# Kernel optimization log

Hardware: AMD Instinct MI355X
Metric: run time of the kernel (lower is better)

Reference implementation:

```python
import jax, jax.numpy as jnp
import numpy as np

B, N, M = 8, 4096, 77
Q_DIM, CTX_DIM = 1024, 768
H, D = 16, 64
INNER = H * D  # 1024


def setup_inputs() -> dict:
    key = jax.random.key(0)
    ks = jax.random.split(key, 7)
    x = jax.random.normal(ks[0], (B, N, Q_DIM), dtype=jnp.float32)
    context = jax.random.normal(ks[1], (B, M, CTX_DIM), dtype=jnp.float32)
    # Linear weights stored as [in, out] so y = x @ W (no bias for q/k/v).
    Wq = jax.random.normal(ks[2], (Q_DIM, INNER), dtype=jnp.float32) * (Q_DIM ** -0.5)
    Wk = jax.random.normal(ks[3], (CTX_DIM, INNER), dtype=jnp.float32) * (CTX_DIM ** -0.5)
    Wv = jax.random.normal(ks[4], (CTX_DIM, INNER), dtype=jnp.float32) * (CTX_DIM ** -0.5)
    Wo = jax.random.normal(ks[5], (INNER, Q_DIM), dtype=jnp.float32) * (INNER ** -0.5)
    bo = jax.random.normal(ks[6], (Q_DIM,), dtype=jnp.float32) * 0.01
    return {"x": x, "context": context, "Wq": Wq, "Wk": Wk, "Wv": Wv, "Wo": Wo, "bo": bo}


def reference(x, context, Wq, Wk, Wv, Wo, bo):
    scale = D ** -0.5
    # Project and split heads: [B, S, H*D] -> [B, H, S, D]
    def heads(t):
        b, s, _ = t.shape
        return t.reshape(b, s, H, D).transpose(0, 2, 1, 3)
    q = heads(x @ Wq)        # [B, H, N, D]
    k = heads(context @ Wk)  # [B, H, M, D]
    v = heads(context @ Wv)  # [B, H, M, D]
    scores = jnp.einsum('bhid,bhjd->bhij', q, k) * scale  # [B, H, N, M]
    attn = jax.nn.softmax(scores, axis=-1)
    out = jnp.einsum('bhij,bhjd->bhid', attn, v)          # [B, H, N, D]
    out = out.transpose(0, 2, 1, 3).reshape(x.shape[0], x.shape[1], INNER)
    return out @ Wo + bo  # dropout p=0.0 -> identity
```

## Files before the change

kernel.cpp:

```cpp
#include <hip/hip_runtime.h>
#include <hip/hip_bf16.h>

typedef _Float16 f16x8 __attribute__((ext_vector_type(8)));
typedef float f32x4 __attribute__((ext_vector_type(4)));

#define MFMA16(a, b, c) __builtin_amdgcn_mfma_f32_16x16x32_f16(a, b, c, 0, 0, 0)

__device__ __forceinline__ void load_lds16(const void* g, void* l) {
  __builtin_amdgcn_global_load_lds(
      (__attribute__((address_space(1))) void*)g,
      (__attribute__((address_space(3))) void*)l, 16, 0, 0);
}

__global__ __launch_bounds__(256) void k_cvt16(const float* __restrict__ in,
                                               _Float16* __restrict__ out, int n8) {
  int stride = gridDim.x * blockDim.x;
  for (int i = blockIdx.x * blockDim.x + threadIdx.x; i < n8; i += stride) {
    const float4* p = (const float4*)(in + (size_t)i * 8);
    float4 a = p[0], b = p[1];
    f16x8 v = {(_Float16)a.x, (_Float16)a.y, (_Float16)a.z, (_Float16)a.w,
               (_Float16)b.x, (_Float16)b.y, (_Float16)b.z, (_Float16)b.w};
    *(f16x8*)(out + (size_t)i * 8) = v;
  }
}

__global__ __launch_bounds__(256) void k_transpose(const float* __restrict__ in,
                                                   _Float16* __restrict__ out, int K, int N) {
  __shared__ float tile[64][65];
  int k0 = blockIdx.y * 64, n0 = blockIdx.x * 64;
  int t = threadIdx.x;
  {
    int nn = t & 63, kb = t >> 6;
#pragma unroll
    for (int i = 0; i < 16; ++i) {
      int kk = kb + i * 4;
      tile[kk][nn] = in[(size_t)(k0 + kk) * N + n0 + nn];
    }
  }
  __syncthreads();
  {
    int kk = t & 63, nb = t >> 6;
#pragma unroll
    for (int i = 0; i < 16; ++i) {
      int nn = nb + i * 4;
      out[(size_t)(n0 + nn) * K + k0 + kk] = (_Float16)tile[kk][nn];
    }
  }
}

__global__ __launch_bounds__(64) void k_kvproj(const _Float16* __restrict__ ctxh,
                                               const _Float16* __restrict__ Wkt,
                                               const _Float16* __restrict__ Wvt,
                                               _Float16* __restrict__ Kg,
                                               _Float16* __restrict__ Vtg) {
  int mt = blockIdx.x, nt = blockIdx.y;
  int lane = threadIdx.x;
  int l15 = lane & 15, lhi = lane >> 4;
  int arow = mt * 16 + l15;
  if (arow > 615) arow = 615;
  const _Float16* ap = ctxh + (size_t)arow * 768 + lhi * 8;
  const _Float16* kp = Wkt + (size_t)(nt * 16 + l15) * 768 + lhi * 8;
  const _Float16* vp = Wvt + (size_t)(nt * 16 + l15) * 768 + lhi * 8;
  f32x4 ak = {0.f, 0.f, 0.f, 0.f}, av = {0.f, 0.f, 0.f, 0.f};
#pragma unroll 4
  for (int ks = 0; ks < 24; ++ks) {
    f16x8 a = *(const f16x8*)(ap + ks * 32);
    f16x8 bk = *(const f16x8*)(kp + ks * 32);
    f16x8 bv = *(const f16x8*)(vp + ks * 32);
    ak = MFMA16(a, bk, ak);
    av = MFMA16(a, bv, av);
  }
  int n = nt * 16 + l15, h = n >> 6, d = n & 63;
#pragma unroll
  for (int j = 0; j < 4; ++j) {
    int gm = mt * 16 + lhi * 4 + j;
    if (gm < 616) {
      int b = gm / 77, m = gm - b * 77;
      Kg[((size_t)(b * 16 + h) * 77 + m) * 64 + d] = (_Float16)ak[j];
      Vtg[((size_t)(b * 16 + h) * 64 + d) * 128 + m] = (_Float16)av[j];
    }
  }
}

__global__ __launch_bounds__(256) void k_attn(const _Float16* __restrict__ Qh,
                                              const _Float16* __restrict__ Kg,
                                              const _Float16* __restrict__ Vtg,
                                              _Float16* __restrict__ Out) {
  __shared__ __align__(16) char Kl[80 * 128];
  __shared__ __align__(16) char Vl[64 * 256];
  __shared__ __align__(16) char Pl[4 * 16 * 256];
  int bh = blockIdx.y, b = bh >> 4, h = bh & 15;
  int t = threadIdx.x, wid = t >> 6, lane = t & 63;
  int l15 = lane & 15, lhi = lane >> 4;

  const _Float16* Kgp = Kg + (size_t)bh * (77 * 64);
  const _Float16* Vgp = Vtg + (size_t)bh * (64 * 128);

  for (int idx = t; idx < 640; idx += 256) {
    int m = idx >> 3, c = (idx & 7) * 8;
    f16x8 v = {};
    if (m < 77) v = *(const f16x8*)(Kgp + m * 64 + c);
    *(f16x8*)(Kl + ((m * 128 + c * 2) ^ ((m & 7) << 4))) = v;
  }
  for (int idx = t; idx < 1024; idx += 256) {
    int d = idx >> 4, c = (idx & 15) * 8;
    f16x8 v = *(const f16x8*)(Vgp + d * 128 + c);
    *(f16x8*)(Vl + ((d * 256 + c * 2) ^ ((d & 7) << 4))) = v;
  }
  char* myP = Pl + wid * 4096;
#pragma unroll
  for (int i = 0; i < 4; ++i) *(f16x8*)(myP + lane * 64 + i * 16) = f16x8{};
  __syncthreads();

  int qrow = b * 4096 + blockIdx.x * 64 + wid * 16 + l15;
  const _Float16* qp = Qh + (size_t)qrow * 1024 + h * 64 + lhi * 8;
  f16x8 q0 = *(const f16x8*)qp;
  f16x8 q1 = *(const f16x8*)(qp + 32);

  float e[5][4];
  float mx[4] = {-1e30f, -1e30f, -1e30f, -1e30f};
#pragma unroll
  for (int ct = 0; ct < 5; ++ct) {
    int m = ct * 16 + l15;
    int d0b = lhi * 16;
    f16x8 k0 = *(const f16x8*)(Kl + ((m * 128 + d0b) ^ ((m & 7) << 4)));
    f16x8 k1 = *(const f16x8*)(Kl + ((m * 128 + 64 + d0b) ^ ((m & 7) << 4)));
    f32x4 acc = {0.f, 0.f, 0.f, 0.f};
    acc = MFMA16(q0, k0, acc);
    acc = MFMA16(q1, k1, acc);
    bool valid = m < 77;
#pragma unroll
    for (int j = 0; j < 4; ++j) {
      float v = valid ? acc[j] * 0.125f : -1e30f;
      e[ct][j] = v;
      mx[j] = fmaxf(mx[j], v);
    }
  }
#pragma unroll
  for (int off = 1; off < 16; off <<= 1)
#pragma unroll
    for (int j = 0; j < 4; ++j) mx[j] = fmaxf(mx[j], __shfl_xor(mx[j], off, 64));
  float sm[4] = {0.f, 0.f, 0.f, 0.f};
#pragma unroll
  for (int ct = 0; ct < 5; ++ct)
#pragma unroll
    for (int j = 0; j < 4; ++j) {
      float ev = __expf(e[ct][j] - mx[j]);
      e[ct][j] = ev;
      sm[j] += ev;
    }
#pragma unroll
  for (int off = 1; off < 16; off <<= 1)
#pragma unroll
    for (int j = 0; j < 4; ++j) sm[j] += __shfl_xor(sm[j], off, 64);
  float rs[4];
#pragma unroll
  for (int j = 0; j < 4; ++j) rs[j] = 1.0f / sm[j];

#pragma unroll
  for (int ct = 0; ct < 5; ++ct) {
    int m = ct * 16 + l15;
#pragma unroll
    for (int j = 0; j < 4; ++j) {
      int r = lhi * 4 + j;
      *(_Float16*)(myP + ((r * 256 + m * 2) ^ ((r & 7) << 4))) =
          (_Float16)(e[ct][j] * rs[j]);
    }
  }

  f32x4 o[4] = {{0.f,0.f,0.f,0.f},{0.f,0.f,0.f,0.f},{0.f,0.f,0.f,0.f},{0.f,0.f,0.f,0.f}};
#pragma unroll
  for (int ks = 0; ks < 3; ++ks) {
    int m0b = ks * 64 + lhi * 16;
    f16x8 pa = *(const f16x8*)(myP + ((l15 * 256 + m0b) ^ ((l15 & 7) << 4)));
#pragma unroll
    for (int dt = 0; dt < 4; ++dt) {
      int d = dt * 16 + l15;
      f16x8 vb = *(const f16x8*)(Vl + ((d * 256 + m0b) ^ ((d & 7) << 4)));
      o[dt] = MFMA16(pa, vb, o[dt]);
    }
  }
  _Float16* op = Out + (size_t)(b * 4096 + blockIdx.x * 64 + wid * 16) * 1024 + h * 64;
#pragma unroll
  for (int dt = 0; dt < 4; ++dt)
#pragma unroll
    for (int j = 0; j < 4; ++j) {
      int r = lhi * 4 + j;
      op[(size_t)r * 1024 + dt * 16 + l15] = (_Float16)o[dt][j];
    }
}

template <int FINAL>
__global__ __launch_bounds__(512, 2) void k_gemm6(const _Float16* __restrict__ A,
                                                  const _Float16* __restrict__ Bt,
                                                  void* __restrict__ Cout,
                                                  const float* __restrict__ bias,
                                                  int M, int N, int K) {
  __shared__ __align__(16) char lds[131072];
  const int t = threadIdx.x, wid = t >> 6, lane = t & 63;
  const int wr = wid >> 2, wc = wid & 3;
  const int l15 = lane & 15, lhi = lane >> 4;

  int nwg = gridDim.x, bid = blockIdx.x;
  int wg = ((nwg & 7) == 0) ? ((bid & 7) * (nwg >> 3) + (bid >> 3)) : bid;
  const int nTN = N >> 8;
  const int tm = wg / nTN, tn = wg % nTN;

  const _Float16* Ag = A + (size_t)tm * 256 * K;
  const _Float16* Bg = Bt + (size_t)tn * 256 * K;
  const size_t stg = (size_t)(wid * 8 + (lane >> 3)) * K +
                     (size_t)(((lane & 7) ^ ((lane >> 3) & 7)) * 8);
  const int dstg = wid * 1024;

  const int x7 = l15 & 7;
  const int cs0 = (lhi ^ x7) << 4;
  const int cs1 = ((4 + lhi) ^ x7) << 4;
  const int aoff = wr * 16384 + l15 * 128;
  const int boff = 32768 + wc * 8192 + l15 * 128;

  f32x4 acc[8][4];
#pragma unroll
  for (int i = 0; i < 8; ++i)
#pragma unroll
    for (int j = 0; j < 4; ++j) acc[i][j] = f32x4{0.f, 0.f, 0.f, 0.f};
  f16x8 a[4][2], b0[2][2], b1[2][2];

#define STG_A(T, RB) load_lds16(Ag + stg + (size_t)(RB) * K + (T) * 64, \
                                lds + ((T) & 1) * 65536 + (RB) * 128 + dstg)
#define STG_B(T, RB) load_lds16(Bg + stg + (size_t)(RB) * K + (T) * 64, \
                                lds + ((T) & 1) * 65536 + 32768 + (RB) * 128 + dstg)
#define RD_A(BUF, MH) { const int p_ = (BUF) * 65536 + aoff + (MH) * 8192;              \
    _Pragma("unroll") for (int mf = 0; mf < 4; ++mf) {                                  \
      a[mf][0] = *(const f16x8*)&lds[p_ + mf * 2048 + cs0];                             \
      a[mf][1] = *(const f16x8*)&lds[p_ + mf * 2048 + cs1]; } }
#define RD_B(BUF, NH, BREG) { const int q_ = (BUF) * 65536 + boff + (NH) * 4096;        \
    _Pragma("unroll") for (int nf = 0; nf < 2; ++nf) {                                  \
      BREG[nf][0] = *(const f16x8*)&lds[q_ + nf * 2048 + cs0];                          \
      BREG[nf][1] = *(const f16x8*)&lds[q_ + nf * 2048 + cs1]; } }
#define MM(MH, NH, BREG) { __builtin_amdgcn_s_setprio(1);                               \
    _Pragma("unroll") for (int mf = 0; mf < 4; ++mf)                                    \
      _Pragma("unroll") for (int nf = 0; nf < 2; ++nf)                                  \
        _Pragma("unroll") for (int kk = 0; kk < 2; ++kk)                                \
          acc[(MH)*4+mf][(NH)*2+nf] = MFMA16(a[mf][kk], BREG[nf][kk],                   \
                                             acc[(MH)*4+mf][(NH)*2+nf]);                \
    __builtin_amdgcn_s_setprio(0); }
#define VM6 asm volatile("s_waitcnt vmcnt(6)" ::: "memory")
#define VM0 asm volatile("s_waitcnt vmcnt(0)" ::: "memory")
#define BAR __builtin_amdgcn_s_barrier()

  const int nT = K >> 6;

  STG_A(0, 0); STG_A(0, 64); STG_A(0, 128); STG_A(0, 192);
  STG_B(0, 0); STG_B(0, 64); STG_B(0, 128); STG_B(0, 192);
  STG_A(1, 0); STG_A(1, 128);
  STG_B(1, 0); STG_B(1, 64); STG_B(1, 128); STG_B(1, 192);
  asm volatile("s_waitcnt vmcnt(6)" ::: "memory");
  BAR;

  const int nPair = (nT - 2) >> 1;
  for (int i = 0; i < nPair; ++i) {
    const int t0 = 2 * i;
    RD_B(0, 0, b0); RD_A(0, 0); STG_A(t0 + 1, 64); STG_A(t0 + 1, 192); BAR; MM(0, 0, b0); BAR;
    RD_B(0, 1, b1); STG_A(t0 + 2, 0); STG_A(t0 + 2, 128); BAR; MM(0, 1, b1); BAR;
    RD_A(0, 1); STG_B(t0 + 2, 0); STG_B(t0 + 2, 64); BAR; MM(1, 1, b1); BAR;
    STG_B(t0 + 2, 128); STG_B(t0 + 2, 192); VM6; BAR; MM(1, 0, b0); BAR;
    RD_B(1, 0, b0); RD_A(1, 0); STG_A(t0 + 2, 64); STG_A(t0 + 2, 192); BAR; MM(0, 0, b0); BAR;
    RD_B(1, 1, b1); STG_A(t0 + 3, 0); STG_A(t0 + 3, 128); BAR; MM(0, 1, b1); BAR;
    RD_A(1, 1); STG_B(t0 + 3, 0); STG_B(t0 + 3, 64); BAR; MM(1, 1, b1); BAR;
    STG_B(t0 + 3, 128); STG_B(t0 + 3, 192); VM6; BAR; MM(1, 0, b0); BAR;
  }
  RD_B(0, 0, b0); RD_A(0, 0); STG_A(nT - 1, 64); STG_A(nT - 1, 192); BAR; MM(0, 0, b0); BAR;
  RD_B(0, 1, b1); BAR; MM(0, 1, b1); BAR;
  RD_A(0, 1); BAR; MM(1, 1, b1); BAR;
  VM0; BAR; MM(1, 0, b0); BAR;
  RD_B(1, 0, b0); RD_A(1, 0); BAR; MM(0, 0, b0); BAR;
  RD_B(1, 1, b1); BAR; MM(0, 1, b1); BAR;
  RD_A(1, 1); BAR; MM(1, 1, b1); BAR;
  MM(1, 0, b0);

  const long rbase = (long)tm * 256 + wr * 128;
  const int cbase = tn * 256 + wc * 64;
#pragma unroll
  for (int mf = 0; mf < 8; ++mf)
#pragma unroll
    for (int nf = 0; nf < 4; ++nf) {
      int c = cbase + nf * 16 + l15;
      float bv = FINAL ? bias[c] : 0.f;
#pragma unroll
      for (int j = 0; j < 4; ++j) {
        long r = rbase + mf * 16 + lhi * 4 + j;
        float v = acc[mf][nf][j];
        if (FINAL) ((float*)Cout)[r * N + c] = v + bv;
        else ((_Float16*)Cout)[r * N + c] = (_Float16)v;
      }
    }
#undef STG_A
#undef STG_B
#undef RD_A
#undef RD_B
#undef MM
#undef VM6
#undef VM0
#undef BAR
}

extern "C" void kernel_launch(void* const* d_in, const int* in_sizes, int n_in,
                              void* d_out, int out_size, void* d_ws, size_t ws_size,
                              hipStream_t stream) {
  const float* x   = (const float*)d_in[0];
  const float* ctx = (const float*)d_in[1];
  const float* Wq  = (const float*)d_in[2];
  const float* Wk  = (const float*)d_in[3];
  const float* Wv  = (const float*)d_in[4];
  const float* Wo  = (const float*)d_in[5];
  const float* bo  = (const float*)d_in[6];

  char* ws = (char*)d_ws;
  _Float16* xh   = (_Float16*)(ws + 0);
  _Float16* Wqt  = (_Float16*)(ws + 67108864);
  _Float16* Wkt  = (_Float16*)(ws + 69206016);
  _Float16* Wvt  = (_Float16*)(ws + 70778880);
  _Float16* Wot  = (_Float16*)(ws + 72351744);
  _Float16* ctxh = (_Float16*)(ws + 74448896);
  _Float16* Kg   = (_Float16*)(ws + 75395072);
  _Float16* Vtg  = (_Float16*)(ws + 76656640);
  _Float16* Qh   = (_Float16*)d_out;

  k_cvt16<<<4096, 256, 0, stream>>>(x, xh, 33554432 / 8);
  k_cvt16<<<231, 256, 0, stream>>>(ctx, ctxh, 473088 / 8);
  k_transpose<<<dim3(16, 16), 256, 0, stream>>>(Wq, Wqt, 1024, 1024);
  k_transpose<<<dim3(16, 12), 256, 0, stream>>>(Wk, Wkt, 768, 1024);
  k_transpose<<<dim3(16, 12), 256, 0, stream>>>(Wv, Wvt, 768, 1024);
  k_transpose<<<dim3(16, 16), 256, 0, stream>>>(Wo, Wot, 1024, 1024);
  hipMemsetAsync(Vtg, 0, 2097152, stream);
  k_kvproj<<<dim3(39, 64), 64, 0, stream>>>(ctxh, Wkt, Wvt, Kg, Vtg);
  k_gemm6<0><<<dim3(512), dim3(512), 0, stream>>>(xh, Wqt, (void*)Qh, nullptr, 32768, 1024, 1024);
  k_attn<<<dim3(64, 128), 256, 0, stream>>>(Qh, Kg, Vtg, xh);
  k_gemm6<1><<<dim3(512), dim3(512), 0, stream>>>(xh, Wot, d_out, bo, 32768, 1024, 1024);
}
```

Measured before the change: 289.7 us.

## Restructure GEMM main loop: one barrier per tile, split-K register fragments

Replaces the GEMM's finely interleaved schedule, which placed a barrier around every MFMA quarter, with a simpler per-tile schedule. Each tile now does a single vmcnt(0) wait plus barrier, issues the whole next-tile prefetch at once, and interleaves LDS fragment reads (split by k-half) with MFMA groups. The aim is to cut barrier overhead and let LDS reads overlap MFMAs within a wave. In exchange, global prefetch is less spread out, the full wait for the next tile may expose load latency, and the extra fragment registers add register pressure.

```diff
diff --git a/kernel.cpp b/kernel.cpp
--- a/kernel.cpp
+++ b/kernel.cpp
@@ -191,7 +191,7 @@
 }
 
 template <int FINAL>
-__global__ __launch_bounds__(512, 2) void k_gemm6(const _Float16* __restrict__ A,
+__global__ __launch_bounds__(512, 2) void k_gemm7(const _Float16* __restrict__ A,
                                                   const _Float16* __restrict__ Bt,
                                                   void* __restrict__ Cout,
                                                   const float* __restrict__ bias,
@@ -223,60 +223,56 @@
   for (int i = 0; i < 8; ++i)
 #pragma unroll
     for (int j = 0; j < 4; ++j) acc[i][j] = f32x4{0.f, 0.f, 0.f, 0.f};
-  f16x8 a[4][2], b0[2][2], b1[2][2];
+  f16x8 a0k0[4], a0k1[4], a1k0[4], a1k1[4];
+  f16x8 b00[2], b01[2], b10[2], b11[2];
 
 #define STG_A(T, RB) load_lds16(Ag + stg + (size_t)(RB) * K + (T) * 64, \
                                 lds + ((T) & 1) * 65536 + (RB) * 128 + dstg)
 #define STG_B(T, RB) load_lds16(Bg + stg + (size_t)(RB) * K + (T) * 64, \
                                 lds + ((T) & 1) * 65536 + 32768 + (RB) * 128 + dstg)
-#define RD_A(BUF, MH) { const int p_ = (BUF) * 65536 + aoff + (MH) * 8192;              \
-    _Pragma("unroll") for (int mf = 0; mf < 4; ++mf) {                                  \
-      a[mf][0] = *(const f16x8*)&lds[p_ + mf * 2048 + cs0];                             \
-      a[mf][1] = *(const f16x8*)&lds[p_ + mf * 2048 + cs1]; } }
-#define RD_B(BUF, NH, BREG) { const int q_ = (BUF) * 65536 + boff + (NH) * 4096;        \
-    _Pragma("unroll") for (int nf = 0; nf < 2; ++nf) {                                  \
-      BREG[nf][0] = *(const f16x8*)&lds[q_ + nf * 2048 + cs0];                          \
-      BREG[nf][1] = *(const f16x8*)&lds[q_ + nf * 2048 + cs1]; } }
-#define MM(MH, NH, BREG) { __builtin_amdgcn_s_setprio(1);                               \
-    _Pragma("unroll") for (int mf = 0; mf < 4; ++mf)                                    \
-      _Pragma("unroll") for (int nf = 0; nf < 2; ++nf)                                  \
-        _Pragma("unroll") for (int kk = 0; kk < 2; ++kk)                                \
-          acc[(MH)*4+mf][(NH)*2+nf] = MFMA16(a[mf][kk], BREG[nf][kk],                   \
-                                             acc[(MH)*4+mf][(NH)*2+nf]);                \
+#define STG_TILE(T) { STG_A(T, 0); STG_A(T, 64); STG_A(T, 128); STG_A(T, 192);  \
+                      STG_B(T, 0); STG_B(T, 64); STG_B(T, 128); STG_B(T, 192); }
+#define RDA(DST, BUF, MH, CS) { const int p_ = (BUF) * 65536 + aoff + (MH) * 8192; \
+    _Pragma("unroll") for (int mf = 0; mf < 4; ++mf)                               \
+      DST[mf] = *(const f16x8*)&lds[p_ + mf * 2048 + (CS)]; }
+#define RDB(DST, BUF, NH, CS) { const int q_ = (BUF) * 65536 + boff + (NH) * 4096; \
+    _Pragma("unroll") for (int nf = 0; nf < 2; ++nf)                               \
+      DST[nf] = *(const f16x8*)&lds[q_ + nf * 2048 + (CS)]; }
+#define MMC(MH, NH, AR, BR) { __builtin_amdgcn_s_setprio(1);                       \
+    _Pragma("unroll") for (int mf = 0; mf < 4; ++mf)                               \
+      _Pragma("unroll") for (int nf = 0; nf < 2; ++nf)                             \
+        acc[(MH)*4+mf][(NH)*2+nf] = MFMA16(AR[mf], BR[nf],                         \
+                                           acc[(MH)*4+mf][(NH)*2+nf]);             \
     __builtin_amdgcn_s_setprio(0); }
-#define VM6 asm volatile("s_waitcnt vmcnt(6)" ::: "memory")
 #define VM0 asm volatile("s_waitcnt vmcnt(0)" ::: "memory")
 #define BAR __builtin_amdgcn_s_barrier()
 
+#define TILE(BUF, T, STG_ON)                                                       \
+  {                                                                                \
+    VM0; BAR;                                                                      \
+    RDA(a0k0, BUF, 0, cs0); RDB(b00, BUF, 0, cs0);                                 \
+    RDB(b10, BUF, 1, cs0);                                                         \
+    if (STG_ON) STG_TILE((T) + 1);                                                 \
+    MMC(0, 0, a0k0, b00);                                                          \
+    RDA(a1k0, BUF, 1, cs0); MMC(0, 1, a0k0, b10);                                  \
+    RDA(a1k1, BUF, 1, cs1); MMC(1, 1, a1k0, b10);                                  \
+    RDB(b01, BUF, 0, cs1);  MMC(1, 0, a1k0, b00);                                  \
+    RDB(b11, BUF, 1, cs1);  MMC(1, 0, a1k1, b01);                                  \
+    RDA(a0k1, BUF, 0, cs1); MMC(1, 1, a1k1, b11);                                  \
+    MMC(0, 1, a0k1, b11);                                                          \
+    MMC(0, 0, a0k1, b01);                                                          \
+  }
+
   const int nT = K >> 6;
 
-  STG_A(0, 0); STG_A(0, 64); STG_A(0, 128); STG_A(0, 192);
-  STG_B(0, 0); STG_B(0, 64); STG_B(0, 128); STG_B(0, 192);
-  STG_A(1, 0); STG_A(1, 128);
-  STG_B(1, 0); STG_B(1, 64); STG_B(1, 128); STG_B(1, 192);
-  asm volatile("s_waitcnt vmcnt(6)" ::: "memory");
-  BAR;
-
-  const int nPair = (nT - 2) >> 1;
-  for (int i = 0; i < nPair; ++i) {
-    const int t0 = 2 * i;
-    RD_B(0, 0, b0); RD_A(0, 0); STG_A(t0 + 1, 64); STG_A(t0 + 1, 192); BAR; MM(0, 0, b0); BAR;
-    RD_B(0, 1, b1); STG_A(t0 + 2, 0); STG_A(t0 + 2, 128); BAR; MM(0, 1, b1); BAR;
-    RD_A(0, 1); STG_B(t0 + 2, 0); STG_B(t0 + 2, 64); BAR; MM(1, 1, b1); BAR;
-    STG_B(t0 + 2, 128); STG_B(t0 + 2, 192); VM6; BAR; MM(1, 0, b0); BAR;
-    RD_B(1, 0, b0); RD_A(1, 0); STG_A(t0 + 2, 64); STG_A(t0 + 2, 192); BAR; MM(0, 0, b0); BAR;
-    RD_B(1, 1, b1); STG_A(t0 + 3, 0); STG_A(t0 + 3, 128); BAR; MM(0, 1, b1); BAR;
-    RD_A(1, 1); STG_B(t0 + 3, 0); STG_B(t0 + 3, 64); BAR; MM(1, 1, b1); BAR;
-    STG_B(t0 + 3, 128); STG_B(t0 + 3, 192); VM6; BAR; MM(1, 0, b0); BAR;
-  }
-  RD_B(0, 0, b0); RD_A(0, 0); STG_A(nT - 1, 64); STG_A(nT - 1, 192); BAR; MM(0, 0, b0); BAR;
-  RD_B(0, 1, b1); BAR; MM(0, 1, b1); BAR;
-  RD_A(0, 1); BAR; MM(1, 1, b1); BAR;
-  VM0; BAR; MM(1, 0, b0); BAR;
-  RD_B(1, 0, b0); RD_A(1, 0); BAR; MM(0, 0, b0); BAR;
-  RD_B(1, 1, b1); BAR; MM(0, 1, b1); BAR;
-  RD_A(1, 1); BAR; MM(1, 1, b1); BAR;
-  MM(1, 0, b0);
+  STG_TILE(0);
+
+  for (int i = 0; i < (nT >> 1) - 1; ++i) {
+    TILE(0, 2 * i, true);
+    TILE(1, 2 * i + 1, true);
+  }
+  TILE(0, nT - 2, true);
+  TILE(1, nT - 1, false);
 
   const long rbase = (long)tm * 256 + wr * 128;
   const int cbase = tn * 256 + wc * 64;
@@ -296,10 +292,11 @@
     }
 #undef STG_A
 #undef STG_B
-#undef RD_A
-#undef RD_B
-#undef MM
-#undef VM6
+#undef STG_TILE
+#undef RDA
+#undef RDB
+#undef MMC
+#undef TILE
 #undef VM0
 #undef BAR
 }
@@ -334,7 +331,7 @@
   k_transpose<<<dim3(16, 16), 256, 0, stream>>>(Wo, Wot, 1024, 1024);
   hipMemsetAsync(Vtg, 0, 2097152, stream);
   k_kvproj<<<dim3(39, 64), 64, 0, stream>>>(ctxh, Wkt, Wvt, Kg, Vtg);
-  k_gemm6<0><<<dim3(512), dim3(512), 0, stream>>>(xh, Wqt, (void*)Qh, nullptr, 32768, 1024, 1024);
+  k_gemm7<0><<<dim3(512), dim3(512), 0, stream>>>(xh, Wqt, (void*)Qh, nullptr, 32768, 1024, 1024);
   k_attn<<<dim3(64, 128), 256, 0, stream>>>(Qh, Kg, Vtg, xh);
-  k_gemm6<1><<<dim3(512), dim3(512), 0, stream>>>(xh, Wot, d_out, bo, 32768, 1024, 1024);
-}
+  k_gemm7<1><<<dim3(512), dim3(512), 0, stream>>>(xh, Wot, d_out, bo, 32768, 1024, 1024);
+}
```

Result: no change. 284.6 us (-1.8%).
